# Kernel optimization log

Measured on AMD Instinct MI355X. Metric: run time of the kernel, lower is better.

Reference implementation:

```python
import jax, jax.numpy as jnp
import numpy as np

A = 9            # cfg.anchors.num
K = 1000         # cfg.frcnn.nms.output_size
IOU_THR = 0.7    # cfg.frcnn.nms.iou
NEG = jnp.float32(-1e30)


def setup_inputs() -> dict:
    key = jax.random.key(0)
    ks = jax.random.split(key, 8)
    B, H, W, C = 1, 100, 152, 1024
    feat = jax.random.normal(ks[0], (B, H, W, C), jnp.float32)
    # conv kernels with small (0.01) std, matching typical RPN truncated-normal init
    w_cls = jax.random.normal(ks[1], (C, 2 * A), jnp.float32) * 0.01
    b_cls = jnp.zeros((2 * A,), jnp.float32)
    w_bbox = jax.random.normal(ks[2], (C, 4 * A), jnp.float32) * 0.01
    b_bbox = jnp.zeros((4 * A,), jnp.float32)
    img_sz = jnp.array([800.0, 1216.0], jnp.float32)
    N = B * H * W * A  # 136800 anchors, [x0, y0, x1, y1]
    cx = jax.random.uniform(ks[3], (N,), jnp.float32, 0.0, 800.0)
    cy = jax.random.uniform(ks[4], (N,), jnp.float32, 0.0, 1216.0)
    sh = jax.random.uniform(ks[5], (N,), jnp.float32, 16.0, 128.0)
    sw = jax.random.uniform(ks[6], (N,), jnp.float32, 16.0, 128.0)
    anchors = jnp.stack([cx - 0.5 * sh, cy - 0.5 * sw, cx + 0.5 * sh, cy + 0.5 * sw], axis=1)
    return {"rpn_feature": feat, "anchors": anchors, "img_sz": img_sz,
            "w_cls": w_cls, "b_cls": b_cls, "w_bbox": w_bbox, "b_bbox": b_bbox}


def convert_and_clip(anchors, pred, img_sz):
    # anchors [N,4]; decode deltas (tx pairs with h, ty with w, per original code)
    w = anchors[:, 3] - anchors[:, 1] + 1.0
    h = anchors[:, 2] - anchors[:, 0] + 1.0
    x = anchors[:, 0] + 0.5 * h
    y = anchors[:, 1] + 0.5 * w
    tx, ty, tw, th = pred[:, 0], pred[:, 1], pred[:, 2], pred[:, 3]
    x_pred = tx * h + x
    y_pred = ty * w + y
    w_pred = jnp.exp(tw) * w
    h_pred = jnp.exp(th) * h
    x0 = jnp.maximum(x_pred - 0.5 * h_pred, 0.0)
    x1 = jnp.minimum(x_pred + 0.5 * h_pred, img_sz[0])
    y0 = jnp.maximum(y_pred - 0.5 * w_pred, 0.0)
    y1 = jnp.minimum(y_pred + 0.5 * w_pred, img_sz[1])
    return jnp.stack([x0, y0, x1, y1], axis=1)


def greedy_nms(boxes, scores, k, iou_thr):
    # boxes [N,4] = [c0, c1, c2, c3]; IoU is symmetric in coord convention
    x0, y0, x1, y1 = boxes[:, 0], boxes[:, 1], boxes[:, 2], boxes[:, 3]
    areas = (x1 - x0) * (y1 - y0)

    def step(s, _):
        i = jnp.argmax(s)
        valid = s[i] > NEG * 0.5
        iw = jnp.maximum(jnp.minimum(x1, x1[i]) - jnp.maximum(x0, x0[i]), 0.0)
        ih = jnp.maximum(jnp.minimum(y1, y1[i]) - jnp.maximum(y0, y0[i]), 0.0)
        inter = iw * ih
        iou = inter / (areas + areas[i] - inter + 1e-9)
        s = jnp.where((iou >= iou_thr) & valid, NEG, s)
        s = s.at[i].set(NEG)
        return s, (i, valid)

    _, (idx, valid) = jax.lax.scan(step, scores, None, length=k)
    return idx, valid


def reference(rpn_feature, anchors, img_sz, w_cls, b_cls, w_bbox, b_bbox):
    # 1x1 convs == per-pixel GEMM
    cls_score = jnp.einsum('bhwc,co->bhwo', rpn_feature, w_cls) + b_cls       # [B,H,W,2A]
    cls_prob2 = jax.nn.softmax(cls_score.reshape(-1, 2), axis=-1)             # pairwise softmax
    cls_pred = jnp.argmax(cls_prob2, axis=-1)
    cls_prob = cls_prob2.reshape(cls_score.shape)
    bbox_pred = (jnp.einsum('bhwc,co->bhwo', rpn_feature, w_bbox) + b_bbox).reshape(-1, 4)
    fg = cls_prob[:, :, :, A:].reshape(-1)                                    # foreground scores
    boxes = convert_and_clip(anchors, bbox_pred, img_sz)                      # [N,4]
    idx, valid = greedy_nms(boxes, fg, K, IOU_THR)
    proposals = jnp.where(valid[:, None], boxes[idx], 0.0)                    # [K,4]
    return proposals, idx, cls_prob, cls_pred, bbox_pred
```

## Files before the change

kernel.cpp:

```cpp
#include <hip/hip_runtime.h>
#include <cstdint>
#include <cstddef>

#define NPOS   15200
#define NANCH  136800
#define KDIM   1024
#define NCLS   18
#define NBB    36
#define KS     8
#define KCH    (KDIM / KS)
#define KSTEP  32
#define MTILE  128
#define MCAP   4096
#define NROW   2048
#define NWRD   32
#define TARGET_SEL 3072
#define KSEL   1000
#define HBINS  8192

typedef unsigned long long u64;

#define OFF_PROP    0
#define OFF_IDX     4000
#define OFF_CLSPROB 5000
#define OFF_CLSPRED 278600
#define OFF_BB      415400

struct Ctrl {
  int selCount;
  int bstar;
  int pad[14];
};

__device__ inline unsigned int fkey(float f) {
  unsigned int b = __float_as_uint(f);
  return (b & 0x80000000u) ? ~b : (b | 0x80000000u);
}

__global__ __launch_bounds__(256) void gemm5(const float* __restrict__ feat,
                                             const float* __restrict__ wcls,
                                             const float* __restrict__ wbb,
                                             double* __restrict__ diffPart,
                                             float* __restrict__ clsPart,
                                             float* __restrict__ bbPart) {
  __shared__ __align__(16) float  fS[KSTEP * MTILE];
  __shared__ __align__(16) float  wL[KCH * 72];
  __shared__ __align__(16) double wDL[KCH * 10];
  const int t = threadIdx.x;
  const int lane = t & 63;
  const int wv   = t >> 6;
  const int P0 = blockIdx.x * MTILE;
  const int k0 = blockIdx.y * KCH;

  for (int idx = t; idx < KCH * NCLS; idx += 256) {
    int k = idx / NCLS, c = idx % NCLS;
    wL[k * 72 + c] = wcls[(size_t)(k0 + k) * NCLS + c];
  }
  for (int idx = t; idx < KCH * NBB; idx += 256) {
    int k = idx / NBB, c = idx % NBB;
    wL[k * 72 + ((c < 18) ? (24 + c) : (48 + (c - 18)))] = wbb[(size_t)(k0 + k) * NBB + c];
  }
  for (int idx = t; idx < KCH * 9; idx += 256) {
    int k = idx / 9, j = idx % 9;
    int cC = 9 + j, cD = cC ^ 1;
    wDL[k * 10 + j] = (double)wcls[(size_t)(k0 + k) * NCLS + cC] -
                      (double)wcls[(size_t)(k0 + k) * NCLS + cD];
  }

  double accd[2][9];
  float  accf[2][18];
#pragma unroll
  for (int p = 0; p < 2; ++p) {
#pragma unroll
    for (int j = 0; j < 9; ++j) accd[p][j] = 0.0;
#pragma unroll
    for (int c = 0; c < 18; ++c) accf[p][c] = 0.f;
  }

  float4 fr[4];
  auto LOADF = [&](int kb) {
#pragma unroll
    for (int j = 0; j < 4; ++j) {
      int idx = j * 256 + t;
      int p = idx >> 3, q = idx & 7;
      int gp = P0 + p;
      fr[j] = make_float4(0.f, 0.f, 0.f, 0.f);
      if (gp < NPOS) fr[j] = *(const float4*)(feat + (size_t)gp * KDIM + kb + q * 4);
    }
  };
  auto WRITEF = [&]() {
#pragma unroll
    for (int j = 0; j < 4; ++j) {
      int idx = j * 256 + t;
      int p = idx >> 3, q = idx & 7;
      const float vv[4] = {fr[j].x, fr[j].y, fr[j].z, fr[j].w};
#pragma unroll
      for (int i = 0; i < 4; ++i) {
        int kk = q * 4 + i;
        int swz = ((kk >> 2) & 7) << 2;
        fS[kk * MTILE + (p ^ swz)] = vv[i];
      }
    }
  };

  LOADF(k0);
  const int NSTEP = KCH / KSTEP;
  for (int s = 0; s < NSTEP; ++s) {
    __syncthreads();
    WRITEF();
    if (s + 1 < NSTEP) LOADF(k0 + (s + 1) * KSTEP);
    __syncthreads();

    const int kb = s * KSTEP;
    if (wv == 0) {
#pragma unroll 4
      for (int kk = 0; kk < KSTEP; ++kk) {
        int swz = ((kk >> 2) & 7) << 2;
        const float2 f2 = *(const float2*)&fS[kk * MTILE + ((lane * 2) ^ swz)];
        double f0 = (double)f2.x, f1 = (double)f2.y;
        const double* wd = &wDL[(kb + kk) * 10];
        const double2 w01 = *(const double2*)&wd[0];
        const double2 w23 = *(const double2*)&wd[2];
        const double2 w45 = *(const double2*)&wd[4];
        const double2 w67 = *(const double2*)&wd[6];
        const double  w8  = wd[8];
        const double w[9] = {w01.x, w01.y, w23.x, w23.y, w45.x, w45.y, w67.x, w67.y, w8};
#pragma unroll
        for (int j = 0; j < 9; ++j) {
          accd[0][j] += f0 * w[j];
          accd[1][j] += f1 * w[j];
        }
      }
    } else {
      const int cb = (wv == 1) ? 0 : ((wv == 2) ? 24 : 48);
#pragma unroll 4
      for (int kk = 0; kk < KSTEP; ++kk) {
        int swz = ((kk >> 2) & 7) << 2;
        const float2 f2 = *(const float2*)&fS[kk * MTILE + ((lane * 2) ^ swz)];
        float f0 = f2.x, f1 = f2.y;
        const float* wp = &wL[(kb + kk) * 72 + cb];
        const float4 w0 = *(const float4*)&wp[0];
        const float4 w1 = *(const float4*)&wp[4];
        const float4 w2 = *(const float4*)&wp[8];
        const float4 w3 = *(const float4*)&wp[12];
        const float2 w4 = *(const float2*)&wp[16];
        const float w[18] = {w0.x, w0.y, w0.z, w0.w, w1.x, w1.y, w1.z, w1.w,
                             w2.x, w2.y, w2.z, w2.w, w3.x, w3.y, w3.z, w3.w,
                             w4.x, w4.y};
#pragma unroll
        for (int c = 0; c < 18; ++c) {
          accf[0][c] += f0 * w[c];
          accf[1][c] += f1 * w[c];
        }
      }
    }
  }

#pragma unroll
  for (int i = 0; i < 2; ++i) {
    int gp = P0 + lane * 2 + i;
    if (gp >= NPOS) continue;
    if (wv == 0) {
      double* o = diffPart + ((size_t)blockIdx.y * NPOS + gp) * 9;
#pragma unroll
      for (int j = 0; j < 9; ++j) o[j] = accd[i][j];
    } else if (wv == 1) {
      float* o = clsPart + ((size_t)blockIdx.y * NPOS + gp) * NCLS;
#pragma unroll
      for (int c = 0; c < 18; ++c) o[c] = accf[i][c];
    } else {
      float* o = bbPart + ((size_t)blockIdx.y * NPOS + gp) * NBB + (wv - 2) * 18;
#pragma unroll
      for (int c = 0; c < 18; ++c) o[c] = accf[i][c];
    }
  }
}

__global__ __launch_bounds__(256) void epilogue(const double* __restrict__ diffPart, const float* __restrict__ clsPart,
                         const float* __restrict__ bbPart,
                         const float* __restrict__ bcls, const float* __restrict__ bbb,
                         const float* __restrict__ anchors, const float* __restrict__ imgsz,
                         float* __restrict__ out, double* __restrict__ dkeys,
                         float* __restrict__ bx0, float* __restrict__ by0,
                         float* __restrict__ bx1, float* __restrict__ by1,
                         float* __restrict__ bar, int* __restrict__ hist) {
  __shared__ int hS[HBINS];
  const int t = threadIdx.x;
  for (int i = t; i < HBINS; i += 256) hS[i] = 0;
  __syncthreads();

  int n = blockIdx.x * 256 + t;
  if (n < NANCH) {
    int pos = n / 9, j = n % 9;
    int cA = 2 * j, cB = 2 * j + 1, cC = 9 + j, cD = cC ^ 1;
    float sA = bcls[cA], sB = bcls[cB];
#pragma unroll
    for (int ks = 0; ks < KS; ++ks) {
      const float* pp = clsPart + ((size_t)ks * NPOS + pos) * NCLS;
      sA += pp[cA]; sB += pp[cB];
    }
    double d = (double)bcls[cC] - (double)bcls[cD];
#pragma unroll
    for (int ks = 0; ks < KS; ++ks)
      d += diffPart[((size_t)ks * NPOS + pos) * 9 + j];

    out[OFF_CLSPROB + (size_t)pos * 18 + cA] = 1.0f / (1.0f + expf(sB - sA));
    out[OFF_CLSPROB + (size_t)pos * 18 + cB] = 1.0f / (1.0f + expf(sA - sB));
    out[OFF_CLSPRED + n] = (sB > sA) ? 1.0f : 0.0f;
    dkeys[n] = d;
    atomicAdd(&hS[fkey((float)d) >> 19], 1);

    float tb[4];
#pragma unroll
    for (int m = 0; m < 4; ++m) {
      float s = bbb[4 * j + m];
#pragma unroll
      for (int ks = 0; ks < KS; ++ks)
        s += bbPart[((size_t)ks * NPOS + pos) * NBB + 4 * j + m];
      tb[m] = s;
      out[OFF_BB + (size_t)n * 4 + m] = s;
    }
    float4 a = *(const float4*)(anchors + (size_t)n * 4);
    float w = a.w - a.y + 1.0f;
    float h = a.z - a.x + 1.0f;
    float x = a.x + 0.5f * h;
    float y = a.y + 0.5f * w;
    float xp = tb[0] * h + x;
    float yp = tb[1] * w + y;
    float wp = expf(tb[2]) * w;
    float hp = expf(tb[3]) * h;
    float X0 = fmaxf(xp - 0.5f * hp, 0.f);
    float X1 = fminf(xp + 0.5f * hp, imgsz[0]);
    float Y0 = fmaxf(yp - 0.5f * wp, 0.f);
    float Y1 = fminf(yp + 0.5f * wp, imgsz[1]);
    bx0[n] = X0; by0[n] = Y0; bx1[n] = X1; by1[n] = Y1;
    bar[n] = (X1 - X0) * (Y1 - Y0);
  }

  __syncthreads();
  for (int i = t; i < HBINS; i += 256) {
    int v = hS[i];
    if (v) atomicAdd(&hist[i], v);
  }
}

__global__ void scank(const int* __restrict__ hist, Ctrl* __restrict__ ctrl) {
  __shared__ int hS[HBINS];
  __shared__ int cS[256];
  int t = threadIdx.x;
  for (int i = t; i < HBINS; i += 256) hS[i] = hist[i];
  __syncthreads();
  int s = 0;
  for (int b = 0; b < 32; ++b) s += hS[t * 32 + b];
  cS[t] = s;
  __syncthreads();
  if (t == 0) {
    int acc = 0;
    for (int cb = 255; cb >= 0; --cb) {
      int cs = cS[cb];
      if (acc + cs >= TARGET_SEL || acc + cs > MCAP) {
        int bstar = cb * 32;
        for (int b = cb * 32 + 31; b >= cb * 32; --b) {
          int h = hS[b];
          if (acc + h > MCAP) { bstar = b + 1; break; }
          acc += h;
          if (acc >= TARGET_SEL) { bstar = b; break; }
        }
        ctrl->bstar = bstar;
        return;
      }
      acc += cs;
    }
    ctrl->bstar = 0;
  }
}

__global__ __launch_bounds__(256) void compactk(const double* __restrict__ dkeys, Ctrl* __restrict__ ctrl,
                                                int* __restrict__ sel) {
  __shared__ int wofs[4];
  __shared__ int base;
  const int t = threadIdx.x;
  const int lane = t & 63, wv = t >> 6;
  int n = blockIdx.x * 256 + t;
  bool pick = false;
  if (n < NANCH) {
    unsigned int u = fkey((float)dkeys[n]);
    pick = ((int)(u >> 19) >= ctrl->bstar);
  }
  u64 b = __ballot(pick);
  int wpre = __popcll(b & ((lane == 0) ? 0ull : (~0ull >> (64 - lane))));
  if (lane == 0) wofs[wv] = __popcll(b);
  __syncthreads();
  if (t == 0) {
    int c0 = wofs[0], c1 = wofs[1], c2 = wofs[2], c3 = wofs[3];
    int tot = c0 + c1 + c2 + c3;
    wofs[0] = 0; wofs[1] = c0; wofs[2] = c0 + c1; wofs[3] = c0 + c1 + c2;
    base = tot ? atomicAdd(&ctrl->selCount, tot) : 0;
  }
  __syncthreads();
  if (pick) {
    int slot = base + wofs[wv] + wpre;
    if (slot < MCAP) sel[slot] = n;
  }
}

__global__ __launch_bounds__(256) void rankk(const double* __restrict__ dkeys,
                                             const int* __restrict__ sel,
                                             const Ctrl* __restrict__ ctrl,
                                             int* __restrict__ rank) {
  int C = ctrl->selCount; if (C > MCAP) C = MCAP;
  if ((int)(blockIdx.x << 8) >= C || (int)(blockIdx.y << 8) >= C) return;
  __shared__ double kS[256];
  __shared__ int    iS[256];
  const int t = threadIdx.x;
  int j = blockIdx.y * 256 + t;
  if (j < C) { int n = sel[j]; kS[t] = dkeys[n]; iS[t] = n; }
  else       { kS[t] = -1.0e300; iS[t] = NANCH + j; }
  int i = blockIdx.x * 256 + t;
  double ki; int ii;
  if (i < C) { int n = sel[i]; ki = dkeys[n]; ii = n; }
  else       { ki = -1.0e300; ii = NANCH + i; }
  __syncthreads();
  int cnt = 0;
#pragma unroll 8
  for (int q = 0; q < 256; ++q) {
    double kq = kS[q]; int iq = iS[q];
    cnt += (int)((kq > ki) || (kq == ki && iq < ii));
  }
  atomicAdd(&rank[i], cnt);
}

__global__ __launch_bounds__(256) void scatterk(const int* __restrict__ sel,
                                                const Ctrl* __restrict__ ctrl,
                                                const int* __restrict__ rank,
                                                int* __restrict__ sidx,
                                                float* __restrict__ sx0, float* __restrict__ sy0,
                                                float* __restrict__ sx1, float* __restrict__ sy1,
                                                float* __restrict__ sar,
                                                const float* __restrict__ bx0, const float* __restrict__ by0,
                                                const float* __restrict__ bx1, const float* __restrict__ by1,
                                                const float* __restrict__ bar) {
  int i = blockIdx.x * 256 + threadIdx.x;
  if (i >= MCAP) return;
  int C = ctrl->selCount;
  if (C > MCAP) C = MCAP;
  if (i < C) {
    int r = rank[i];
    if (r < 0 || r >= MCAP) return;
    int n = sel[i];
    sidx[r] = n;
    sx0[r] = bx0[n]; sy0[r] = by0[n]; sx1[r] = bx1[n]; sy1[r] = by1[n]; sar[r] = bar[n];
  } else {
    sidx[i] = 0x7FFFFFFF;
    sx0[i] = 0.f; sy0[i] = 0.f; sx1[i] = 0.f; sy1[i] = 0.f; sar[i] = 0.f;
  }
}

__global__ __launch_bounds__(256) void iouk2(const float* __restrict__ sx0, const float* __restrict__ sy0,
                                             const float* __restrict__ sx1, const float* __restrict__ sy1,
                                             const float* __restrict__ sar,
                                             u64* __restrict__ mask) {
  __shared__ float X0[NROW], Y0[NROW], X1[NROW], Y1[NROW], AR[NROW];
  int t = threadIdx.x;
  for (int i = t; i < NROW; i += 256) {
    X0[i] = sx0[i]; Y0[i] = sy0[i]; X1[i] = sx1[i]; Y1[i] = sy1[i]; AR[i] = sar[i];
  }
  __syncthreads();
  int r0 = blockIdx.x * 16;
  for (int task = t; task < 16 * NWRD; task += 256) {
    int r = r0 + (task >> 5);
    int w = task & 31;
    float x0r = X0[r], y0r = Y0[r], x1r = X1[r], y1r = Y1[r], arr = AR[r];
    u64 bits = 0ull;
#pragma unroll 16
    for (int jj = 0; jj < 64; ++jj) {
      int jc = (w << 6) + jj;
      float iw = fminf(x1r, X1[jc]) - fmaxf(x0r, X0[jc]);
      iw = fmaxf(iw, 0.f);
      float ih = fminf(y1r, Y1[jc]) - fmaxf(y0r, Y0[jc]);
      ih = fmaxf(ih, 0.f);
      float inter = iw * ih;
      float iou = inter / (AR[jc] + arr - inter + 1e-9f);
      bits |= ((u64)(iou >= 0.7f)) << jj;
    }
    mask[(size_t)r * NWRD + w] = bits;
  }
}

__global__ __launch_bounds__(64) void nmsk2(const u64* __restrict__ mask,
                                            const int* __restrict__ sidx,
                                            const float* __restrict__ sx0, const float* __restrict__ sy0,
                                            const float* __restrict__ sx1, const float* __restrict__ sy1,
                                            const float* __restrict__ sar,
                                            const Ctrl* __restrict__ ctrl,
                                            float* __restrict__ out) {
  __shared__ int keptPos[KSEL];
  const int lane = threadIdx.x;
  const int h = lane >> 5, m = lane & 31;
  int C = ctrl->selCount; if (C > MCAP) C = MCAP;
  int kept = 0;
  u64 sup = 0;
  const int nwin = min((C + 63) >> 6, NROW >> 6);

  u64 bufA[32], bufB[32], dgA = 0, dgB = 0;

  auto ISSUE = [&](u64* buf, u64& dg, int w) {
    const u64* base = mask + ((size_t)(w * 64 + h * 32) * NWRD + m);
#pragma unroll
    for (int j = 0; j < 32; ++j) buf[j] = base[(size_t)j * NWRD];
    dg = mask[((size_t)(w * 64 + lane)) * NWRD + w];
  };

  auto PROCW = [&](u64* buf, u64 dg, int w) {
    u64 swin = __shfl(sup, w);
    int rem = C - w * 64;
    u64 vmask = (rem >= 64) ? ~0ull : ((1ull << rem) - 1);
    u64 cand = (~swin) & vmask;
    u64 keep = 0;
    if (cand) {
      u64 gt = (lane == 63) ? 0ull : (~0ull << (lane + 1));
      bool own = (cand >> lane) & 1;
      u64 bad = __ballot(own && ((dg & cand & gt) != 0ull));
      if (bad == 0ull) {
        keep = cand;
      } else {
        u64 cur = cand;
        for (int j = 0; j < 64; ++j) {
          if ((cur >> j) & 1) {
            keep |= 1ull << j;
            u64 dj = __shfl(dg, j);
            u64 gtj = (j == 63) ? 0ull : (~0ull << (j + 1));
            cur &= ~(dj & gtj);
          }
        }
      }
    }
    int pc = __popcll(keep);
    int need = KSEL - kept;
    while (pc > need) { keep &= ~(1ull << (63 - __clzll(keep))); --pc; }
    if ((keep >> lane) & 1) {
      int p = kept + __popcll(keep & ((1ull << lane) - 1ull));
      keptPos[p] = w * 64 + lane;
    }
    u64 orv = 0;
    u64 kmh = h ? (keep >> 32) : (keep & 0xffffffffull);
#pragma unroll
    for (int j = 0; j < 32; ++j)
      if ((kmh >> j) & 1) orv |= buf[j];
    orv |= __shfl_xor(orv, 32);
    sup |= orv;
    kept += pc;
  };

  if (nwin > 0) {
    ISSUE(bufA, dgA, 0);
    int w = 0;
    while (w < nwin && kept < KSEL) {
      if (w + 1 < nwin) ISSUE(bufB, dgB, w + 1);
      PROCW(bufA, dgA, w); ++w;
      if (w >= nwin || kept >= KSEL) break;
      if (w + 1 < nwin) ISSUE(bufA, dgA, w + 1);
      PROCW(bufB, dgB, w); ++w;
    }
  }

  for (int r = NROW; r < C && kept < KSEL; ++r) {
    float x0 = sx0[r], y0 = sy0[r], x1 = sx1[r], y1 = sy1[r], ar = sar[r];
    bool supr = false;
    for (int b = lane; b < kept; b += 64) {
      int kp = keptPos[b];
      float iw = fminf(x1, sx1[kp]) - fmaxf(x0, sx0[kp]);
      iw = fmaxf(iw, 0.f);
      float ih = fminf(y1, sy1[kp]) - fmaxf(y0, sy0[kp]);
      ih = fmaxf(ih, 0.f);
      float inter = iw * ih;
      float iou = inter / (sar[kp] + ar - inter + 1e-9f);
      if (iou >= 0.7f) supr = true;
    }
    if (__ballot(supr) != 0ull) continue;
    if (lane == 0) keptPos[kept] = r;
    ++kept;
  }

  __syncthreads();
  for (int q = lane; q < KSEL; q += 64) {
    if (q < kept) {
      int kp = keptPos[q];
      int n = sidx[kp];
      out[OFF_PROP + 4 * q + 0] = sx0[kp];
      out[OFF_PROP + 4 * q + 1] = sy0[kp];
      out[OFF_PROP + 4 * q + 2] = sx1[kp];
      out[OFF_PROP + 4 * q + 3] = sy1[kp];
      out[OFF_IDX + q] = (float)n;
    } else {
      out[OFF_PROP + 4 * q + 0] = 0.f;
      out[OFF_PROP + 4 * q + 1] = 0.f;
      out[OFF_PROP + 4 * q + 2] = 0.f;
      out[OFF_PROP + 4 * q + 3] = 0.f;
      out[OFF_IDX + q] = 0.f;
    }
  }
}

__global__ void badws(float* out) {
  if (threadIdx.x == 0 && blockIdx.x == 0) out[0] = 1.0e8f;
}

extern "C" void kernel_launch(void* const* d_in, const int* in_sizes, int n_in,
                              void* d_out, int out_size, void* d_ws, size_t ws_size,
                              hipStream_t stream) {
  (void)in_sizes; (void)n_in; (void)out_size;
  const float* feat    = (const float*)d_in[0];
  const float* anchors = (const float*)d_in[1];
  const float* imgsz   = (const float*)d_in[2];
  const float* wcls    = (const float*)d_in[3];
  const float* bcls    = (const float*)d_in[4];
  const float* wbb     = (const float*)d_in[5];
  const float* bbb     = (const float*)d_in[6];
  float* out = (float*)d_out;
  char* ws = (char*)d_ws;

  const size_t o_diff   = 0;
  const size_t o_cls    = o_diff + (size_t)KS * NPOS * 9 * 8;
  const size_t o_bb     = o_cls + (size_t)KS * NPOS * NCLS * 4;
  const size_t o_dkeys  = o_bb + (size_t)KS * NPOS * NBB * 4;
  const size_t o_bx0    = o_dkeys + (size_t)NANCH * 8;
  const size_t o_by0    = o_bx0 + (size_t)NANCH * 4;
  const size_t o_bx1    = o_by0 + (size_t)NANCH * 4;
  const size_t o_by1    = o_bx1 + (size_t)NANCH * 4;
  const size_t o_bar    = o_by1 + (size_t)NANCH * 4;
  const size_t o_hist   = o_bar + (size_t)NANCH * 4;
  const size_t o_ctrl   = o_hist + (size_t)HBINS * 4;
// ... 4 lines not shown
  const size_t o_sy0    = o_sx0 + (size_t)MCAP * 4;
  const size_t o_sx1    = o_sy0 + (size_t)MCAP * 4;
  const size_t o_sy1    = o_sx1 + (size_t)MCAP * 4;
  const size_t o_sar    = o_sy1 + (size_t)MCAP * 4;
  const size_t o_mask   = o_sar + (size_t)MCAP * 4;
  const size_t need     = o_mask + (size_t)NROW * NWRD * 8;

  if (ws_size < need) {
    badws<<<dim3(1), dim3(64), 0, stream>>>(out);
    return;
  }

  double* diffPart = (double*)(ws + o_diff);
  float*  clsPart  = (float*)(ws + o_cls);
  float*  bbPart   = (float*)(ws + o_bb);
  double* dkeys    = (double*)(ws + o_dkeys);
  float*  bx0      = (float*)(ws + o_bx0);
  float*  by0      = (float*)(ws + o_by0);
  float*  bx1      = (float*)(ws + o_bx1);
  float*  by1      = (float*)(ws + o_by1);
  float*  bar      = (float*)(ws + o_bar);
  int*    hist     = (int*)(ws + o_hist);
  Ctrl*   ctrl     = (Ctrl*)(ws + o_ctrl);
  int*    rank     = (int*)(ws + o_rank);
  int*    sel      = (int*)(ws + o_sel);
  int*    sidx     = (int*)(ws + o_sidx);
  float*  sx0      = (float*)(ws + o_sx0);
  float*  sy0      = (float*)(ws + o_sy0);
  float*  sx1      = (float*)(ws + o_sx1);
  float*  sy1      = (float*)(ws + o_sy1);
  float*  sar      = (float*)(ws + o_sar);
  u64*    mask     = (u64*)(ws + o_mask);

  hipMemsetAsync(ws + o_hist, 0, (size_t)HBINS * 4 + 256 + (size_t)MCAP * 4, stream);

  gemm5<<<dim3((NPOS + MTILE - 1) / MTILE, KS), dim3(256), 0, stream>>>(
      feat, wcls, wbb, diffPart, clsPart, bbPart);
  epilogue<<<dim3((NANCH + 255) / 256), dim3(256), 0, stream>>>(
      diffPart, clsPart, bbPart, bcls, bbb, anchors, imgsz, out, dkeys, bx0, by0, bx1, by1, bar, hist);
  scank<<<dim3(1), dim3(256), 0, stream>>>(hist, ctrl);
  compactk<<<dim3((NANCH + 255) / 256), dim3(256), 0, stream>>>(dkeys, ctrl, sel);
  rankk<<<dim3(MCAP / 256, MCAP / 256), dim3(256), 0, stream>>>(dkeys, sel, ctrl, rank);
  scatterk<<<dim3(MCAP / 256), dim3(256), 0, stream>>>(sel, ctrl, rank, sidx,
                                                       sx0, sy0, sx1, sy1, sar,
                                                       bx0, by0, bx1, by1, bar);
  iouk2<<<dim3(NROW / 16), dim3(256), 0, stream>>>(sx0, sy0, sx1, sy1, sar, mask);
  nmsk2<<<dim3(1), dim3(64), 0, stream>>>(mask, sidx, sx0, sy0, sx1, sy1, sar, ctrl, out);
}
```

Before: 171.4 us.

## Fuse post-GEMM NMS pipeline into one cooperative kernel with grid syncs

```diff
diff --git a/kernel.cpp b/kernel.cpp
--- a/kernel.cpp
+++ b/kernel.cpp
@@ -1,4 +1,5 @@
 #include <hip/hip_runtime.h>
+#include <hip/hip_cooperative_groups.h>
 #include <cstdint>
 #include <cstddef>
 
@@ -37,15 +38,14 @@
   return (b & 0x80000000u) ? ~b : (b | 0x80000000u);
 }
 
-__global__ __launch_bounds__(256) void gemm5(const float* __restrict__ feat,
+__global__ __launch_bounds__(256) void gemm8(const float* __restrict__ feat,
                                              const float* __restrict__ wcls,
                                              const float* __restrict__ wbb,
                                              double* __restrict__ diffPart,
                                              float* __restrict__ clsPart,
                                              float* __restrict__ bbPart) {
-  __shared__ __align__(16) float  fS[KSTEP * MTILE];
-  __shared__ __align__(16) float  wL[KCH * 72];
-  __shared__ __align__(16) double wDL[KCH * 10];
+  __shared__ __align__(16) float fS[KSTEP * MTILE];
+  __shared__ __align__(16) float wL[KCH * 60];
   const int t = threadIdx.x;
   const int lane = t & 63;
   const int wv   = t >> 6;
@@ -54,17 +54,11 @@
 
   for (int idx = t; idx < KCH * NCLS; idx += 256) {
     int k = idx / NCLS, c = idx % NCLS;
-    wL[k * 72 + c] = wcls[(size_t)(k0 + k) * NCLS + c];
+    wL[k * 60 + c] = wcls[(size_t)(k0 + k) * NCLS + c];
   }
   for (int idx = t; idx < KCH * NBB; idx += 256) {
     int k = idx / NBB, c = idx % NBB;
-    wL[k * 72 + ((c < 18) ? (24 + c) : (48 + (c - 18)))] = wbb[(size_t)(k0 + k) * NBB + c];
-  }
-  for (int idx = t; idx < KCH * 9; idx += 256) {
-    int k = idx / 9, j = idx % 9;
-    int cC = 9 + j, cD = cC ^ 1;
-    wDL[k * 10 + j] = (double)wcls[(size_t)(k0 + k) * NCLS + cC] -
-                      (double)wcls[(size_t)(k0 + k) * NCLS + cD];
+    wL[k * 60 + ((c < 18) ? (20 + c) : (40 + (c - 18)))] = wbb[(size_t)(k0 + k) * NBB + c];
   }
 
   double accd[2][9];
@@ -118,13 +112,16 @@
         int swz = ((kk >> 2) & 7) << 2;
         const float2 f2 = *(const float2*)&fS[kk * MTILE + ((lane * 2) ^ swz)];
         double f0 = (double)f2.x, f1 = (double)f2.y;
-        const double* wd = &wDL[(kb + kk) * 10];
-        const double2 w01 = *(const double2*)&wd[0];
-        const double2 w23 = *(const double2*)&wd[2];
-        const double2 w45 = *(const double2*)&wd[4];
-        const double2 w67 = *(const double2*)&wd[6];
-        const double  w8  = wd[8];
-        const double w[9] = {w01.x, w01.y, w23.x, w23.y, w45.x, w45.y, w67.x, w67.y, w8};
+        const float* wp = &wL[(kb + kk) * 60];
+        const float4 wA = *(const float4*)&wp[8];
+        const float4 wB = *(const float4*)&wp[12];
+        const float2 wC = *(const float2*)&wp[16];
+        double e0 = (double)wA.y - (double)wA.x;
+        double e1 = (double)wA.z - (double)wA.w;
+        double e2 = (double)wB.x - (double)wB.y;
+        double e3 = (double)wB.z - (double)wB.w;
+        double e4 = (double)wC.x - (double)wC.y;
+        const double w[9] = {e0, e1, -e1, e2, -e2, e3, -e3, e4, -e4};
 #pragma unroll
         for (int j = 0; j < 9; ++j) {
           accd[0][j] += f0 * w[j];
@@ -132,13 +129,13 @@
         }
       }
     } else {
-      const int cb = (wv == 1) ? 0 : ((wv == 2) ? 24 : 48);
+      const int cb = (wv == 1) ? 0 : ((wv == 2) ? 20 : 40);
 #pragma unroll 4
       for (int kk = 0; kk < KSTEP; ++kk) {
         int swz = ((kk >> 2) & 7) << 2;
         const float2 f2 = *(const float2*)&fS[kk * MTILE + ((lane * 2) ^ swz)];
         float f0 = f2.x, f1 = f2.y;
-        const float* wp = &wL[(kb + kk) * 72 + cb];
+        const float* wp = &wL[(kb + kk) * 60 + cb];
         const float4 w0 = *(const float4*)&wp[0];
         const float4 w1 = *(const float4*)&wp[4];
         const float4 w2 = *(const float4*)&wp[8];
@@ -176,200 +173,203 @@
   }
 }
 
-__global__ __launch_bounds__(256) void epilogue(const double* __restrict__ diffPart, const float* __restrict__ clsPart,
-                         const float* __restrict__ bbPart,
-                         const float* __restrict__ bcls, const float* __restrict__ bbb,
-                         const float* __restrict__ anchors, const float* __restrict__ imgsz,
-                         float* __restrict__ out, double* __restrict__ dkeys,
-                         float* __restrict__ bx0, float* __restrict__ by0,
-                         float* __restrict__ bx1, float* __restrict__ by1,
-                         float* __restrict__ bar, int* __restrict__ hist) {
-  __shared__ int hS[HBINS];
+__global__ __launch_bounds__(256) void nmschain(
+    const double* __restrict__ diffPart, const float* __restrict__ clsPart,
+    const float* __restrict__ bbPart, const float* __restrict__ bcls,
+    const float* __restrict__ bbb, const float* __restrict__ anchors,
+    const float* __restrict__ imgsz, float* __restrict__ out,
+    double* __restrict__ dkeys, float* __restrict__ bx0, float* __restrict__ by0,
+    float* __restrict__ bx1, float* __restrict__ by1, float* __restrict__ bar,
+    int* __restrict__ hist, Ctrl* __restrict__ ctrl, int* __restrict__ sel,
+    int* __restrict__ rank, int* __restrict__ sidx,
+    float* __restrict__ sx0, float* __restrict__ sy0, float* __restrict__ sx1,
+    float* __restrict__ sy1, float* __restrict__ sar, u64* __restrict__ mask) {
+  namespace cg = cooperative_groups;
+  cg::grid_group grid = cg::this_grid();
+  __shared__ __align__(16) char shraw[NROW * 5 * 4 + 64];
+  __shared__ int s_bstar, s_wofs[4], s_base, s_kept;
   const int t = threadIdx.x;
-  for (int i = t; i < HBINS; i += 256) hS[i] = 0;
-  __syncthreads();
-
-  int n = blockIdx.x * 256 + t;
-  if (n < NANCH) {
-    int pos = n / 9, j = n % 9;
-    int cA = 2 * j, cB = 2 * j + 1, cC = 9 + j, cD = cC ^ 1;
-    float sA = bcls[cA], sB = bcls[cB];
-#pragma unroll
-    for (int ks = 0; ks < KS; ++ks) {
-      const float* pp = clsPart + ((size_t)ks * NPOS + pos) * NCLS;
-      sA += pp[cA]; sB += pp[cB];
-    }
-    double d = (double)bcls[cC] - (double)bcls[cD];
-#pragma unroll
-    for (int ks = 0; ks < KS; ++ks)
-      d += diffPart[((size_t)ks * NPOS + pos) * 9 + j];
-
-    out[OFF_CLSPROB + (size_t)pos * 18 + cA] = 1.0f / (1.0f + expf(sB - sA));
-    out[OFF_CLSPROB + (size_t)pos * 18 + cB] = 1.0f / (1.0f + expf(sA - sB));
-    out[OFF_CLSPRED + n] = (sB > sA) ? 1.0f : 0.0f;
-    dkeys[n] = d;
-    atomicAdd(&hS[fkey((float)d) >> 19], 1);
-
-    float tb[4];
-#pragma unroll
-    for (int m = 0; m < 4; ++m) {
-      float s = bbb[4 * j + m];
-#pragma unroll
-      for (int ks = 0; ks < KS; ++ks)
-        s += bbPart[((size_t)ks * NPOS + pos) * NBB + 4 * j + m];
-      tb[m] = s;
-      out[OFF_BB + (size_t)n * 4 + m] = s;
-    }
-    float4 a = *(const float4*)(anchors + (size_t)n * 4);
-    float w = a.w - a.y + 1.0f;
-    float h = a.z - a.x + 1.0f;
-    float x = a.x + 0.5f * h;
-    float y = a.y + 0.5f * w;
-    float xp = tb[0] * h + x;
-    float yp = tb[1] * w + y;
-    float wp = expf(tb[2]) * w;
-    float hp = expf(tb[3]) * h;
-    float X0 = fmaxf(xp - 0.5f * hp, 0.f);
-    float X1 = fminf(xp + 0.5f * hp, imgsz[0]);
-    float Y0 = fmaxf(yp - 0.5f * wp, 0.f);
-    float Y1 = fminf(yp + 0.5f * wp, imgsz[1]);
-    bx0[n] = X0; by0[n] = Y0; bx1[n] = X1; by1[n] = Y1;
-    bar[n] = (X1 - X0) * (Y1 - Y0);
-  }
-
-  __syncthreads();
-  for (int i = t; i < HBINS; i += 256) {
-    int v = hS[i];
-    if (v) atomicAdd(&hist[i], v);
-  }
-}
-
-__global__ void scank(const int* __restrict__ hist, Ctrl* __restrict__ ctrl) {
-  __shared__ int hS[HBINS];
-  __shared__ int cS[256];
-  int t = threadIdx.x;
-  for (int i = t; i < HBINS; i += 256) hS[i] = hist[i];
-  __syncthreads();
-  int s = 0;
-  for (int b = 0; b < 32; ++b) s += hS[t * 32 + b];
-  cS[t] = s;
-  __syncthreads();
-  if (t == 0) {
-    int acc = 0;
-    for (int cb = 255; cb >= 0; --cb) {
-      int cs = cS[cb];
-      if (acc + cs >= TARGET_SEL || acc + cs > MCAP) {
-        int bstar = cb * 32;
-        for (int b = cb * 32 + 31; b >= cb * 32; --b) {
-          int h = hS[b];
-          if (acc + h > MCAP) { bstar = b + 1; break; }
-          acc += h;
-          if (acc >= TARGET_SEL) { bstar = b; break; }
-        }
-        ctrl->bstar = bstar;
-        return;
-      }
-      acc += cs;
-    }
-    ctrl->bstar = 0;
-  }
-}
-
-__global__ __launch_bounds__(256) void compactk(const double* __restrict__ dkeys, Ctrl* __restrict__ ctrl,
-                                                int* __restrict__ sel) {
-  __shared__ int wofs[4];
-  __shared__ int base;
-  const int t = threadIdx.x;
-  const int lane = t & 63, wv = t >> 6;
-  int n = blockIdx.x * 256 + t;
-  bool pick = false;
-  if (n < NANCH) {
-    unsigned int u = fkey((float)dkeys[n]);
-    pick = ((int)(u >> 19) >= ctrl->bstar);
-  }
-  u64 b = __ballot(pick);
-  int wpre = __popcll(b & ((lane == 0) ? 0ull : (~0ull >> (64 - lane))));
-  if (lane == 0) wofs[wv] = __popcll(b);
-  __syncthreads();
-  if (t == 0) {
-    int c0 = wofs[0], c1 = wofs[1], c2 = wofs[2], c3 = wofs[3];
-    int tot = c0 + c1 + c2 + c3;
-    wofs[0] = 0; wofs[1] = c0; wofs[2] = c0 + c1; wofs[3] = c0 + c1 + c2;
-    base = tot ? atomicAdd(&ctrl->selCount, tot) : 0;
-  }
-  __syncthreads();
-  if (pick) {
-    int slot = base + wofs[wv] + wpre;
-    if (slot < MCAP) sel[slot] = n;
-  }
-}
-
-__global__ __launch_bounds__(256) void rankk(const double* __restrict__ dkeys,
-                                             const int* __restrict__ sel,
-                                             const Ctrl* __restrict__ ctrl,
-                                             int* __restrict__ rank) {
-  int C = ctrl->selCount; if (C > MCAP) C = MCAP;
-  if ((int)(blockIdx.x << 8) >= C || (int)(blockIdx.y << 8) >= C) return;
-  __shared__ double kS[256];
-  __shared__ int    iS[256];
-  const int t = threadIdx.x;
-  int j = blockIdx.y * 256 + t;
-  if (j < C) { int n = sel[j]; kS[t] = dkeys[n]; iS[t] = n; }
-  else       { kS[t] = -1.0e300; iS[t] = NANCH + j; }
-  int i = blockIdx.x * 256 + t;
-  double ki; int ii;
-  if (i < C) { int n = sel[i]; ki = dkeys[n]; ii = n; }
-  else       { ki = -1.0e300; ii = NANCH + i; }
-  __syncthreads();
-  int cnt = 0;
+  const int b = blockIdx.x;
+  const int NB = gridDim.x;
+  const int lane = t & 63, wvi = t >> 6;
+
+  {
+    int* hS = (int*)shraw;
+    for (int i = t; i < HBINS; i += 256) hS[i] = 0;
+    __syncthreads();
+    for (int base = b * 256; base < NANCH; base += NB * 256) {
+      int n = base + t;
+      if (n < NANCH) {
+        int pos = n / 9, j = n % 9;
+        int cA = 2 * j, cB = 2 * j + 1, cC = 9 + j, cD = cC ^ 1;
+        float sA = bcls[cA], sB = bcls[cB];
+#pragma unroll
+        for (int ks = 0; ks < KS; ++ks) {
+          const float* pp = clsPart + ((size_t)ks * NPOS + pos) * NCLS;
+          sA += pp[cA]; sB += pp[cB];
+        }
+        double d = (double)bcls[cC] - (double)bcls[cD];
+#pragma unroll
+        for (int ks = 0; ks < KS; ++ks)
+          d += diffPart[((size_t)ks * NPOS + pos) * 9 + j];
+
+        out[OFF_CLSPROB + (size_t)pos * 18 + cA] = 1.0f / (1.0f + expf(sB - sA));
+        out[OFF_CLSPROB + (size_t)pos * 18 + cB] = 1.0f / (1.0f + expf(sA - sB));
+        out[OFF_CLSPRED + n] = (sB > sA) ? 1.0f : 0.0f;
+        dkeys[n] = d;
+        atomicAdd(&hS[fkey((float)d) >> 19], 1);
+
+        float tb[4];
+#pragma unroll
+        for (int m = 0; m < 4; ++m) {
+          float s = bbb[4 * j + m];
+#pragma unroll
+          for (int ks = 0; ks < KS; ++ks)
+            s += bbPart[((size_t)ks * NPOS + pos) * NBB + 4 * j + m];
+          tb[m] = s;
+          out[OFF_BB + (size_t)n * 4 + m] = s;
+        }
+        float4 a = *(const float4*)(anchors + (size_t)n * 4);
+        float w = a.w - a.y + 1.0f;
+        float h = a.z - a.x + 1.0f;
+        float x = a.x + 0.5f * h;
+        float y = a.y + 0.5f * w;
+        float xp = tb[0] * h + x;
+        float yp = tb[1] * w + y;
+        float wp = expf(tb[2]) * w;
+        float hp = expf(tb[3]) * h;
+        float X0 = fmaxf(xp - 0.5f * hp, 0.f);
+        float X1 = fminf(xp + 0.5f * hp, imgsz[0]);
+        float Y0 = fmaxf(yp - 0.5f * wp, 0.f);
+        float Y1 = fminf(yp + 0.5f * wp, imgsz[1]);
+        bx0[n] = X0; by0[n] = Y0; bx1[n] = X1; by1[n] = Y1;
+        bar[n] = (X1 - X0) * (Y1 - Y0);
+      }
+    }
+    __syncthreads();
+    for (int i = t; i < HBINS; i += 256) {
+      int v = hS[i];
+      if (v) atomicAdd(&hist[i], v);
+    }
+  }
+  grid.sync();
+
+  {
+    int* hS = (int*)shraw;
+    int* cS = (int*)(shraw + HBINS * 4);
+    for (int i = t; i < HBINS; i += 256) hS[i] = hist[i];
+    __syncthreads();
+    int s = 0;
+    for (int q = 0; q < 32; ++q) s += hS[t * 32 + q];
+    cS[t] = s;
+    __syncthreads();
+    if (t == 0) {
+      int acc = 0, bstar = 0;
+      for (int cb = 255; cb >= 0; --cb) {
+        int cs = cS[cb];
+        if (acc + cs >= TARGET_SEL || acc + cs > MCAP) {
+          bstar = cb * 32;
+          for (int bb2 = cb * 32 + 31; bb2 >= cb * 32; --bb2) {
+            int h = hS[bb2];
+            if (acc + h > MCAP) { bstar = bb2 + 1; break; }
+            acc += h;
+            if (acc >= TARGET_SEL) { bstar = bb2; break; }
+          }
+          break;
+        }
+        acc += cs;
+      }
+      s_bstar = bstar;
+    }
+    __syncthreads();
+  }
+
+  {
+    const int bstar = s_bstar;
+    for (int base = b * 256; base < NANCH; base += NB * 256) {
+      __syncthreads();
+      int n = base + t;
+      bool pick = false;
+      if (n < NANCH) {
+        unsigned int u = fkey((float)dkeys[n]);
+        pick = ((int)(u >> 19) >= bstar);
+      }
+      u64 bm = __ballot(pick);
+      int wpre = __popcll(bm & ((lane == 0) ? 0ull : (~0ull >> (64 - lane))));
+      if (lane == 0) s_wofs[wvi] = __popcll(bm);
+      __syncthreads();
+      if (t == 0) {
+        int c0 = s_wofs[0], c1 = s_wofs[1], c2 = s_wofs[2], c3 = s_wofs[3];
+        int tot = c0 + c1 + c2 + c3;
+        s_wofs[0] = 0; s_wofs[1] = c0; s_wofs[2] = c0 + c1; s_wofs[3] = c0 + c1 + c2;
+        s_base = tot ? atomicAdd(&ctrl->selCount, tot) : 0;
+      }
+      __syncthreads();
+      if (pick) {
+        int slot = s_base + s_wofs[wvi] + wpre;
+        if (slot < MCAP) sel[slot] = n;
+      }
+    }
+  }
+  grid.sync();
+
+  {
+    int C = ctrl->selCount; if (C > MCAP) C = MCAP;
+    int bx = b & 15, by = b >> 4;
+    if ((bx << 8) < C && (by << 8) < C) {
+      double* kS = (double*)shraw;
+      int*    iS = (int*)(shraw + 2048);
+      int j = by * 256 + t;
+      if (j < C) { int n = sel[j]; kS[t] = dkeys[n]; iS[t] = n; }
+      else       { kS[t] = -1.0e300; iS[t] = NANCH + j; }
+      int i = bx * 256 + t;
+      double ki; int ii;
+      if (i < C) { int n = sel[i]; ki = dkeys[n]; ii = n; }
+      else       { ki = -1.0e300; ii = NANCH + i; }
+      __syncthreads();
+      int cnt = 0;
 #pragma unroll 8
-  for (int q = 0; q < 256; ++q) {
-    double kq = kS[q]; int iq = iS[q];
-    cnt += (int)((kq > ki) || (kq == ki && iq < ii));
-  }
-  atomicAdd(&rank[i], cnt);
-}
-
-__global__ __launch_bounds__(256) void scatterk(const int* __restrict__ sel,
-                                                const Ctrl* __restrict__ ctrl,
-                                                const int* __restrict__ rank,
-                                                int* __restrict__ sidx,
-                                                float* __restrict__ sx0, float* __restrict__ sy0,
-                                                float* __restrict__ sx1, float* __restrict__ sy1,
-                                                float* __restrict__ sar,
-                                                const float* __restrict__ bx0, const float* __restrict__ by0,
-                                                const float* __restrict__ bx1, const float* __restrict__ by1,
-                                                const float* __restrict__ bar) {
-  int i = blockIdx.x * 256 + threadIdx.x;
-  if (i >= MCAP) return;
-  int C = ctrl->selCount;
-  if (C > MCAP) C = MCAP;
-  if (i < C) {
-    int r = rank[i];
-    if (r < 0 || r >= MCAP) return;
-    int n = sel[i];
-    sidx[r] = n;
-    sx0[r] = bx0[n]; sy0[r] = by0[n]; sx1[r] = bx1[n]; sy1[r] = by1[n]; sar[r] = bar[n];
-  } else {
-    sidx[i] = 0x7FFFFFFF;
-    sx0[i] = 0.f; sy0[i] = 0.f; sx1[i] = 0.f; sy1[i] = 0.f; sar[i] = 0.f;
-  }
-}
-
-__global__ __launch_bounds__(256) void iouk2(const float* __restrict__ sx0, const float* __restrict__ sy0,
-                                             const float* __restrict__ sx1, const float* __restrict__ sy1,
-                                             const float* __restrict__ sar,
-                                             u64* __restrict__ mask) {
-  __shared__ float X0[NROW], Y0[NROW], X1[NROW], Y1[NROW], AR[NROW];
-  int t = threadIdx.x;
-  for (int i = t; i < NROW; i += 256) {
-    X0[i] = sx0[i]; Y0[i] = sy0[i]; X1[i] = sx1[i]; Y1[i] = sy1[i]; AR[i] = sar[i];
-  }
-  __syncthreads();
-  int r0 = blockIdx.x * 16;
-  for (int task = t; task < 16 * NWRD; task += 256) {
-    int r = r0 + (task >> 5);
-    int w = task & 31;
+      for (int q = 0; q < 256; ++q) {
+        double kq = kS[q]; int iq = iS[q];
+        cnt += (int)((kq > ki) || (kq == ki && iq < ii));
+      }
+      atomicAdd(&rank[i], cnt);
+    }
+  }
+  grid.sync();
+
+  {
+    int C = ctrl->selCount; if (C > MCAP) C = MCAP;
+    int i = b * 256 + t;
+    if (i < MCAP) {
+      if (i < C) {
+        int r = rank[i];
+        if (r >= 0 && r < MCAP) {
+          int n = sel[i];
+          sidx[r] = n;
+          sx0[r] = bx0[n]; sy0[r] = by0[n]; sx1[r] = bx1[n]; sy1[r] = by1[n]; sar[r] = bar[n];
+        }
+      } else {
+        sidx[i] = 0x7FFFFFFF;
+        sx0[i] = 0.f; sy0[i] = 0.f; sx1[i] = 0.f; sy1[i] = 0.f; sar[i] = 0.f;
+      }
+    }
+  }
+  grid.sync();
+
+  {
+    float* X0 = (float*)shraw;
+    float* Y0 = (float*)(shraw + NROW * 4);
+    float* X1 = (float*)(shraw + NROW * 8);
+    float* Y1 = (float*)(shraw + NROW * 12);
+    float* AR = (float*)(shraw + NROW * 16);
+    __syncthreads();
+    for (int i = t; i < NROW; i += 256) {
+      X0[i] = sx0[i]; Y0[i] = sy0[i]; X1[i] = sx1[i]; Y1[i] = sy1[i]; AR[i] = sar[i];
+    }
+    __syncthreads();
+    int r = b * 8 + (t >> 5);
+    int w = t & 31;
     float x0r = X0[r], y0r = Y0[r], x1r = X1[r], y1r = Y1[r], arr = AR[r];
     u64 bits = 0ull;
 #pragma unroll 16
@@ -385,119 +385,113 @@
     }
     mask[(size_t)r * NWRD + w] = bits;
   }
-}
-
-__global__ __launch_bounds__(64) void nmsk2(const u64* __restrict__ mask,
-                                            const int* __restrict__ sidx,
-                                            const float* __restrict__ sx0, const float* __restrict__ sy0,
-                                            const float* __restrict__ sx1, const float* __restrict__ sy1,
-                                            const float* __restrict__ sar,
-                                            const Ctrl* __restrict__ ctrl,
-                                            float* __restrict__ out) {
-  __shared__ int keptPos[KSEL];
-  const int lane = threadIdx.x;
-  const int h = lane >> 5, m = lane & 31;
-  int C = ctrl->selCount; if (C > MCAP) C = MCAP;
-  int kept = 0;
-  u64 sup = 0;
-  const int nwin = min((C + 63) >> 6, NROW >> 6);
-
-  u64 bufA[32], bufB[32], dgA = 0, dgB = 0;
-
-  auto ISSUE = [&](u64* buf, u64& dg, int w) {
-    const u64* base = mask + ((size_t)(w * 64 + h * 32) * NWRD + m);
-#pragma unroll
-    for (int j = 0; j < 32; ++j) buf[j] = base[(size_t)j * NWRD];
-    dg = mask[((size_t)(w * 64 + lane)) * NWRD + w];
-  };
-
-  auto PROCW = [&](u64* buf, u64 dg, int w) {
-    u64 swin = __shfl(sup, w);
-    int rem = C - w * 64;
-    u64 vmask = (rem >= 64) ? ~0ull : ((1ull << rem) - 1);
-    u64 cand = (~swin) & vmask;
-    u64 keep = 0;
-    if (cand) {
-      u64 gt = (lane == 63) ? 0ull : (~0ull << (lane + 1));
-      bool own = (cand >> lane) & 1;
-      u64 bad = __ballot(own && ((dg & cand & gt) != 0ull));
-      if (bad == 0ull) {
-        keep = cand;
+  grid.sync();
+
+  if (b == 0) {
+    int* keptPos = (int*)shraw;
+    int C = ctrl->selCount; if (C > MCAP) C = MCAP;
+    if (t < 64) {
+      const int h = lane >> 5, m = lane & 31;
+      int kept = 0;
+      u64 sup = 0;
+      const int nwin = min((C + 63) >> 6, NROW >> 6);
+      u64 bufA[32], bufB[32], dgA = 0, dgB = 0;
+
+      auto ISSUE = [&](u64* buf, u64& dg, int w) {
+        const u64* base2 = mask + ((size_t)(w * 64 + h * 32) * NWRD + m);
+#pragma unroll
+        for (int j = 0; j < 32; ++j) buf[j] = base2[(size_t)j * NWRD];
+        dg = mask[((size_t)(w * 64 + lane)) * NWRD + w];
+      };
+      auto PROCW = [&](u64* buf, u64 dg, int w) {
+        u64 swin = __shfl(sup, w);
+        int rem = C - w * 64;
+        u64 vmask = (rem >= 64) ? ~0ull : ((1ull << rem) - 1);
+        u64 cand = (~swin) & vmask;
+        u64 keep = 0;
+        if (cand) {
+          u64 gt = (lane == 63) ? 0ull : (~0ull << (lane + 1));
+          bool own = (cand >> lane) & 1;
+          u64 bad = __ballot(own && ((dg & cand & gt) != 0ull));
+          if (bad == 0ull) {
+            keep = cand;
+          } else {
+            u64 cur = cand;
+            for (int j = 0; j < 64; ++j) {
+              if ((cur >> j) & 1) {
+                keep |= 1ull << j;
+                u64 dj = __shfl(dg, j);
+                u64 gtj = (j == 63) ? 0ull : (~0ull << (j + 1));
+                cur &= ~(dj & gtj);
+              }
+            }
+          }
+        }
+        int pc = __popcll(keep);
+        int need = KSEL - kept;
+        while (pc > need) { keep &= ~(1ull << (63 - __clzll(keep))); --pc; }
+        if ((keep >> lane) & 1) {
+          int p = kept + __popcll(keep & ((1ull << lane) - 1ull));
+          keptPos[p] = w * 64 + lane;
+        }
+        u64 orv = 0;
+        u64 kmh = h ? (keep >> 32) : (keep & 0xffffffffull);
+#pragma unroll
+        for (int j = 0; j < 32; ++j)
+          if ((kmh >> j) & 1) orv |= buf[j];
+        orv |= __shfl_xor(orv, 32);
+        sup |= orv;
+        kept += pc;
+      };
+
+      if (nwin > 0) {
+        ISSUE(bufA, dgA, 0);
+        int w = 0;
+        while (w < nwin && kept < KSEL) {
+          if (w + 1 < nwin) ISSUE(bufB, dgB, w + 1);
+          PROCW(bufA, dgA, w); ++w;
+          if (w >= nwin || kept >= KSEL) break;
+          if (w + 1 < nwin) ISSUE(bufA, dgA, w + 1);
+          PROCW(bufB, dgB, w); ++w;
+        }
+      }
+      for (int r = NROW; r < C && kept < KSEL; ++r) {
+        float x0 = sx0[r], y0 = sy0[r], x1 = sx1[r], y1 = sy1[r], ar = sar[r];
+        bool supr = false;
+        for (int q = lane; q < kept; q += 64) {
+          int kp = keptPos[q];
+          float iw = fminf(x1, sx1[kp]) - fmaxf(x0, sx0[kp]);
+          iw = fmaxf(iw, 0.f);
+          float ih = fminf(y1, sy1[kp]) - fmaxf(y0, sy0[kp]);
+          ih = fmaxf(ih, 0.f);
+          float inter = iw * ih;
+          float iou = inter / (sar[kp] + ar - inter + 1e-9f);
+          if (iou >= 0.7f) supr = true;
+        }
+        if (__ballot(supr) != 0ull) continue;
+        if (lane == 0) keptPos[kept] = r;
+        ++kept;
+      }
+      if (lane == 0) s_kept = kept;
+    }
+    __syncthreads();
+    int kept = s_kept;
+    for (int q = t; q < KSEL; q += 256) {
+      if (q < kept) {
+        int kp = keptPos[q];
+        int n = sidx[kp];
+        out[OFF_PROP + 4 * q + 0] = sx0[kp];
+        out[OFF_PROP + 4 * q + 1] = sy0[kp];
+        out[OFF_PROP + 4 * q + 2] = sx1[kp];
+        out[OFF_PROP + 4 * q + 3] = sy1[kp];
+        out[OFF_IDX + q] = (float)n;
       } else {
-        u64 cur = cand;
-        for (int j = 0; j < 64; ++j) {
-          if ((cur >> j) & 1) {
-            keep |= 1ull << j;
-            u64 dj = __shfl(dg, j);
-            u64 gtj = (j == 63) ? 0ull : (~0ull << (j + 1));
-            cur &= ~(dj & gtj);
-          }
-        }
-      }
-    }
-    int pc = __popcll(keep);
-    int need = KSEL - kept;
-    while (pc > need) { keep &= ~(1ull << (63 - __clzll(keep))); --pc; }
-    if ((keep >> lane) & 1) {
-      int p = kept + __popcll(keep & ((1ull << lane) - 1ull));
-      keptPos[p] = w * 64 + lane;
-    }
-    u64 orv = 0;
-    u64 kmh = h ? (keep >> 32) : (keep & 0xffffffffull);
-#pragma unroll
-    for (int j = 0; j < 32; ++j)
-      if ((kmh >> j) & 1) orv |= buf[j];
-    orv |= __shfl_xor(orv, 32);
-    sup |= orv;
-    kept += pc;
-  };
-
-  if (nwin > 0) {
-    ISSUE(bufA, dgA, 0);
-    int w = 0;
-    while (w < nwin && kept < KSEL) {
-      if (w + 1 < nwin) ISSUE(bufB, dgB, w + 1);
-      PROCW(bufA, dgA, w); ++w;
-      if (w >= nwin || kept >= KSEL) break;
-      if (w + 1 < nwin) ISSUE(bufA, dgA, w + 1);
-      PROCW(bufB, dgB, w); ++w;
-    }
-  }
-
-  for (int r = NROW; r < C && kept < KSEL; ++r) {
-    float x0 = sx0[r], y0 = sy0[r], x1 = sx1[r], y1 = sy1[r], ar = sar[r];
-    bool supr = false;
-    for (int b = lane; b < kept; b += 64) {
-      int kp = keptPos[b];
-      float iw = fminf(x1, sx1[kp]) - fmaxf(x0, sx0[kp]);
-      iw = fmaxf(iw, 0.f);
-      float ih = fminf(y1, sy1[kp]) - fmaxf(y0, sy0[kp]);
-      ih = fmaxf(ih, 0.f);
-      float inter = iw * ih;
-      float iou = inter / (sar[kp] + ar - inter + 1e-9f);
-      if (iou >= 0.7f) supr = true;
-    }
-    if (__ballot(supr) != 0ull) continue;
-    if (lane == 0) keptPos[kept] = r;
-    ++kept;
-  }
-
-  __syncthreads();
-  for (int q = lane; q < KSEL; q += 64) {
-    if (q < kept) {
-      int kp = keptPos[q];
-      int n = sidx[kp];
-      out[OFF_PROP + 4 * q + 0] = sx0[kp];
-      out[OFF_PROP + 4 * q + 1] = sy0[kp];
-      out[OFF_PROP + 4 * q + 2] = sx1[kp];
-      out[OFF_PROP + 4 * q + 3] = sy1[kp];
-      out[OFF_IDX + q] = (float)n;
-    } else {
-      out[OFF_PROP + 4 * q + 0] = 0.f;
-      out[OFF_PROP + 4 * q + 1] = 0.f;
-      out[OFF_PROP + 4 * q + 2] = 0.f;
-      out[OFF_PROP + 4 * q + 3] = 0.f;
-      out[OFF_IDX + q] = 0.f;
+        out[OFF_PROP + 4 * q + 0] = 0.f;
+        out[OFF_PROP + 4 * q + 1] = 0.f;
+        out[OFF_PROP + 4 * q + 2] = 0.f;
+        out[OFF_PROP + 4 * q + 3] = 0.f;
+        out[OFF_IDX + q] = 0.f;
+      }
     }
   }
 }
@@ -570,16 +564,15 @@
 
   hipMemsetAsync(ws + o_hist, 0, (size_t)HBINS * 4 + 256 + (size_t)MCAP * 4, stream);
 
-  gemm5<<<dim3((NPOS + MTILE - 1) / MTILE, KS), dim3(256), 0, stream>>>(
+  gemm8<<<dim3((NPOS + MTILE - 1) / MTILE, KS), dim3(256), 0, stream>>>(
       feat, wcls, wbb, diffPart, clsPart, bbPart);
-  epilogue<<<dim3((NANCH + 255) / 256), dim3(256), 0, stream>>>(
-      diffPart, clsPart, bbPart, bcls, bbb, anchors, imgsz, out, dkeys, bx0, by0, bx1, by1, bar, hist);
-  scank<<<dim3(1), dim3(256), 0, stream>>>(hist, ctrl);
-  compactk<<<dim3((NANCH + 255) / 256), dim3(256), 0, stream>>>(dkeys, ctrl, sel);
-  rankk<<<dim3(MCAP / 256, MCAP / 256), dim3(256), 0, stream>>>(dkeys, sel, ctrl, rank);
-  scatterk<<<dim3(MCAP / 256), dim3(256), 0, stream>>>(sel, ctrl, rank, sidx,
-                                                       sx0, sy0, sx1, sy1, sar,
-                                                       bx0, by0, bx1, by1, bar);
-  iouk2<<<dim3(NROW / 16), dim3(256), 0, stream>>>(sx0, sy0, sx1, sy1, sar, mask);
-  nmsk2<<<dim3(1), dim3(64), 0, stream>>>(mask, sidx, sx0, sy0, sx1, sy1, sar, ctrl, out);
+
+  void* args[] = {
+    (void*)&diffPart, (void*)&clsPart, (void*)&bbPart, (void*)&bcls, (void*)&bbb,
+    (void*)&anchors, (void*)&imgsz, (void*)&out, (void*)&dkeys,
+    (void*)&bx0, (void*)&by0, (void*)&bx1, (void*)&by1, (void*)&bar,
+    (void*)&hist, (void*)&ctrl, (void*)&sel, (void*)&rank, (void*)&sidx,
+    (void*)&sx0, (void*)&sy0, (void*)&sx1, (void*)&sy1, (void*)&sar, (void*)&mask
+  };
+  hipLaunchCooperativeKernel((const void*)nmschain, dim3(256), dim3(256), args, 0, stream);
 }
```

Measured after the change: 293.4 us. +71.1%, slower.

## Stage GEMM weights in halves, fold workspace zeroing into GEMM, parallelize scan

Applied to the files above, without the earlier changes.

```diff
diff --git a/kernel.cpp b/kernel.cpp
--- a/kernel.cpp
+++ b/kernel.cpp
@@ -11,12 +11,14 @@
 #define KCH    (KDIM / KS)
 #define KSTEP  32
 #define MTILE  128
+#define WHALF  64
 #define MCAP   4096
 #define NROW   2048
 #define NWRD   32
 #define TARGET_SEL 3072
 #define KSEL   1000
 #define HBINS  8192
+#define ZWORDS ((HBINS * 4 + 256 + MCAP * 4) / 4)
 
 typedef unsigned long long u64;
 
@@ -37,35 +39,43 @@
   return (b & 0x80000000u) ? ~b : (b | 0x80000000u);
 }
 
-__global__ __launch_bounds__(256) void gemm5(const float* __restrict__ feat,
-                                             const float* __restrict__ wcls,
-                                             const float* __restrict__ wbb,
-                                             double* __restrict__ diffPart,
-                                             float* __restrict__ clsPart,
-                                             float* __restrict__ bbPart) {
+__global__ __launch_bounds__(256) void gemm10(const float* __restrict__ feat,
+                                              const float* __restrict__ wcls,
+                                              const float* __restrict__ wbb,
+                                              double* __restrict__ diffPart,
+                                              float* __restrict__ clsPart,
+                                              float* __restrict__ bbPart,
+                                              int* __restrict__ zbase) {
   __shared__ __align__(16) float  fS[KSTEP * MTILE];
-  __shared__ __align__(16) float  wL[KCH * 72];
-  __shared__ __align__(16) double wDL[KCH * 10];
+  __shared__ __align__(16) float  wL[WHALF * 60];
+  __shared__ __align__(16) double wDL[WHALF * 10];
   const int t = threadIdx.x;
   const int lane = t & 63;
   const int wv   = t >> 6;
   const int P0 = blockIdx.x * MTILE;
   const int k0 = blockIdx.y * KCH;
 
-  for (int idx = t; idx < KCH * NCLS; idx += 256) {
-    int k = idx / NCLS, c = idx % NCLS;
-    wL[k * 72 + c] = wcls[(size_t)(k0 + k) * NCLS + c];
-  }
-  for (int idx = t; idx < KCH * NBB; idx += 256) {
-    int k = idx / NBB, c = idx % NBB;
-    wL[k * 72 + ((c < 18) ? (24 + c) : (48 + (c - 18)))] = wbb[(size_t)(k0 + k) * NBB + c];
-  }
-  for (int idx = t; idx < KCH * 9; idx += 256) {
-    int k = idx / 9, j = idx % 9;
-    int cC = 9 + j, cD = cC ^ 1;
-    wDL[k * 10 + j] = (double)wcls[(size_t)(k0 + k) * NCLS + cC] -
-                      (double)wcls[(size_t)(k0 + k) * NCLS + cD];
-  }
+  if (blockIdx.x == 0 && blockIdx.y == 0) {
+    for (int i = t; i < ZWORDS; i += 256) zbase[i] = 0;
+  }
+
+  auto STAGEW = [&](int half) {
+    const int kb = k0 + half * WHALF;
+    for (int idx = t; idx < WHALF * NCLS; idx += 256) {
+      int k = idx / NCLS, c = idx % NCLS;
+      wL[k * 60 + c] = wcls[(size_t)(kb + k) * NCLS + c];
+    }
+    for (int idx = t; idx < WHALF * NBB; idx += 256) {
+      int k = idx / NBB, c = idx % NBB;
+      wL[k * 60 + ((c < 18) ? (20 + c) : (40 + (c - 18)))] = wbb[(size_t)(kb + k) * NBB + c];
+    }
+    for (int idx = t; idx < WHALF * 9; idx += 256) {
+      int k = idx / 9, j = idx % 9;
+      int cC = 9 + j, cD = cC ^ 1;
+      wDL[k * 10 + j] = (double)wcls[(size_t)(kb + k) * NCLS + cC] -
+                        (double)wcls[(size_t)(kb + k) * NCLS + cD];
+    }
+  };
 
   double accd[2][9];
   float  accf[2][18];
@@ -108,17 +118,18 @@
   for (int s = 0; s < NSTEP; ++s) {
     __syncthreads();
     WRITEF();
+    if ((s & 1) == 0) STAGEW(s >> 1);
     if (s + 1 < NSTEP) LOADF(k0 + (s + 1) * KSTEP);
     __syncthreads();
 
-    const int kb = s * KSTEP;
+    const int lb = (s & 1) * KSTEP;
     if (wv == 0) {
 #pragma unroll 4
       for (int kk = 0; kk < KSTEP; ++kk) {
         int swz = ((kk >> 2) & 7) << 2;
         const float2 f2 = *(const float2*)&fS[kk * MTILE + ((lane * 2) ^ swz)];
         double f0 = (double)f2.x, f1 = (double)f2.y;
-        const double* wd = &wDL[(kb + kk) * 10];
+        const double* wd = &wDL[(lb + kk) * 10];
         const double2 w01 = *(const double2*)&wd[0];
         const double2 w23 = *(const double2*)&wd[2];
         const double2 w45 = *(const double2*)&wd[4];
@@ -132,13 +143,13 @@
         }
       }
     } else {
-      const int cb = (wv == 1) ? 0 : ((wv == 2) ? 24 : 48);
+      const int cb = (wv == 1) ? 0 : ((wv == 2) ? 20 : 40);
 #pragma unroll 4
       for (int kk = 0; kk < KSTEP; ++kk) {
         int swz = ((kk >> 2) & 7) << 2;
         const float2 f2 = *(const float2*)&fS[kk * MTILE + ((lane * 2) ^ swz)];
         float f0 = f2.x, f1 = f2.y;
-        const float* wp = &wL[(kb + kk) * 72 + cb];
+        const float* wp = &wL[(lb + kk) * 60 + cb];
         const float4 w0 = *(const float4*)&wp[0];
         const float4 w1 = *(const float4*)&wp[4];
         const float4 w2 = *(const float4*)&wp[8];
@@ -244,34 +255,35 @@
   }
 }
 
-__global__ void scank(const int* __restrict__ hist, Ctrl* __restrict__ ctrl) {
+__global__ __launch_bounds__(256) void scank(const int* __restrict__ hist, Ctrl* __restrict__ ctrl) {
   __shared__ int hS[HBINS];
-  __shared__ int cS[256];
-  int t = threadIdx.x;
+  __shared__ int sufS[256];
+  const int t = threadIdx.x;
   for (int i = t; i < HBINS; i += 256) hS[i] = hist[i];
   __syncthreads();
   int s = 0;
+#pragma unroll
   for (int b = 0; b < 32; ++b) s += hS[t * 32 + b];
-  cS[t] = s;
-  __syncthreads();
-  if (t == 0) {
-    int acc = 0;
-    for (int cb = 255; cb >= 0; --cb) {
-      int cs = cS[cb];
-      if (acc + cs >= TARGET_SEL || acc + cs > MCAP) {
-        int bstar = cb * 32;
-        for (int b = cb * 32 + 31; b >= cb * 32; --b) {
-          int h = hS[b];
-          if (acc + h > MCAP) { bstar = b + 1; break; }
-          acc += h;
-          if (acc >= TARGET_SEL) { bstar = b; break; }
-        }
-        ctrl->bstar = bstar;
-        return;
-      }
-      acc += cs;
-    }
-    ctrl->bstar = 0;
+  sufS[t] = s;
+  __syncthreads();
+  for (int off = 1; off < 256; off <<= 1) {
+    int v = (t + off < 256) ? sufS[t + off] : 0;
+    __syncthreads();
+    sufS[t] += v;
+    __syncthreads();
+  }
+  int Ftop = (t + 1 < 256) ? sufS[t + 1] : 0;
+  int Fbot = sufS[t];
+  if (Ftop < TARGET_SEL && Fbot >= TARGET_SEL) {
+    int acc = Ftop;
+    int bstar = t * 32;
+    for (int b = t * 32 + 31; b >= t * 32; --b) {
+      int h = hS[b];
+      if (acc + h > MCAP) { bstar = b + 1; break; }
+      acc += h;
+      if (acc >= TARGET_SEL) { bstar = b; break; }
+    }
+    ctrl->bstar = bstar;
   }
 }
 
@@ -568,10 +580,8 @@
   float*  sar      = (float*)(ws + o_sar);
   u64*    mask     = (u64*)(ws + o_mask);
 
-  hipMemsetAsync(ws + o_hist, 0, (size_t)HBINS * 4 + 256 + (size_t)MCAP * 4, stream);
-
-  gemm5<<<dim3((NPOS + MTILE - 1) / MTILE, KS), dim3(256), 0, stream>>>(
-      feat, wcls, wbb, diffPart, clsPart, bbPart);
+  gemm10<<<dim3((NPOS + MTILE - 1) / MTILE, KS), dim3(256), 0, stream>>>(
+      feat, wcls, wbb, diffPart, clsPart, bbPart, (int*)(ws + o_hist));
   epilogue<<<dim3((NANCH + 255) / 256), dim3(256), 0, stream>>>(
       diffPart, clsPart, bbPart, bcls, bbb, anchors, imgsz, out, dkeys, bx0, by0, bx1, by1, bar, hist);
   scank<<<dim3(1), dim3(256), 0, stream>>>(hist, ctrl);
```

Result: slower. 176.9 us (+3.2%).
